# Performance work log

Hardware: AMD Instinct MI355X
Metric: run time of the kernel (lower is better)

The kernel has to match this reference:

```python
import jax, jax.numpy as jnp
import numpy as np

DIM = 512
HEADS = 8
HEAD_DIM = DIM // HEADS
R = 2  # reduce_ratio
SCALE = HEAD_DIM ** -0.5


def setup_inputs() -> dict:
    key = jax.random.key(0)
    ks = jax.random.split(key, 8)
    bs, H, W = 4, 64, 64
    n = H * W
    std = 0.02
    x = jax.random.normal(ks[0], (bs, n, DIM), dtype=jnp.float32)
    q_w = jax.random.normal(ks[1], (DIM, DIM), dtype=jnp.float32) * std
    kv_w = jax.random.normal(ks[2], (DIM, 2 * DIM), dtype=jnp.float32) * std
    proj_w = jax.random.normal(ks[3], (DIM, DIM), dtype=jnp.float32) * std
    proj_b = jnp.zeros((DIM,), dtype=jnp.float32)
    # Conv2d(dim, dim, kernel=R, stride=R), kaiming-like init
    fan_out = R * R * DIM
    sr_w = jax.random.normal(ks[4], (DIM, DIM, R, R), dtype=jnp.float32) * np.sqrt(2.0 / fan_out)
    sr_b = jnp.zeros((DIM,), dtype=jnp.float32)
    ln_w = jnp.ones((DIM,), dtype=jnp.float32)
    ln_b = jnp.zeros((DIM,), dtype=jnp.float32)
    return {"x": x, "q_w": q_w, "kv_w": kv_w, "proj_w": proj_w, "proj_b": proj_b,
            "sr_w": sr_w, "sr_b": sr_b, "ln_w": ln_w, "ln_b": ln_b, "H": H, "W": W}


def _layernorm(x, w, b, eps=1e-5):
    mu = jnp.mean(x, axis=-1, keepdims=True)
    var = jnp.var(x, axis=-1, keepdims=True)
    return (x - mu) * jax.lax.rsqrt(var + eps) * w + b


def reference(x, q_w, kv_w, proj_w, proj_b, sr_w, sr_b, ln_w, ln_b, H, W):
    bs, n, ch = x.shape
    # q: (bs, heads, n, head_dim)
    q = (x @ q_w).reshape(bs, n, HEADS, HEAD_DIM).transpose(0, 2, 1, 3)
    # spatial reduction of kv source: strided conv + layernorm
    x_img = x.transpose(0, 2, 1).reshape(bs, ch, H, W)
    xr = jax.lax.conv_general_dilated(
        x_img, sr_w, window_strides=(R, R), padding='VALID',
        dimension_numbers=('NCHW', 'OIHW', 'NCHW')) + sr_b[None, :, None, None]
    xr = xr.reshape(bs, ch, -1).transpose(0, 2, 1)  # (bs, n_kv, ch)
    xr = _layernorm(xr, ln_w, ln_b)
    kv = xr @ kv_w  # (bs, n_kv, 2*ch)
    n_kv = kv.shape[1]
    kv = kv.reshape(bs, n_kv, 2, HEADS, HEAD_DIM).transpose(2, 0, 3, 1, 4)
    k, v = kv[0], kv[1]  # (bs, heads, n_kv, head_dim)
    att = jnp.einsum('bhqd,bhkd->bhqk', q, k) * SCALE
    att = jax.nn.softmax(att, axis=-1)
    net = jnp.einsum('bhqk,bhkd->bhqd', att, v)
    net = net.transpose(0, 2, 1, 3).reshape(bs, n, ch)
    return net @ proj_w + proj_b
```

## Files before the change

kernel.cpp:

```cpp
#include <hip/hip_runtime.h>
#include <cstdint>

#define HEADS 8
#define HD 64
#define NQ 4096
#define NKV 1024

typedef unsigned short u16;
typedef __attribute__((ext_vector_type(8))) short short8;
typedef __attribute__((ext_vector_type(4))) float f32x4;
typedef __attribute__((ext_vector_type(16))) float f32x16;

__device__ __forceinline__ u16 f2bf(float f){
  union { float f; unsigned u; } c; c.f = f;
  unsigned r = c.u + 0x7fffu + ((c.u >> 16) & 1u);
  return (u16)(r >> 16);
}
__device__ __forceinline__ unsigned pack2(float a, float b){
  return (unsigned)f2bf(a) | ((unsigned)f2bf(b) << 16);
}
__device__ __forceinline__ float fexp2(float x){
  float r;
  asm("v_exp_f32 %0, %1" : "=v"(r) : "v"(x));
  return r;
}
__device__ __forceinline__ unsigned cvtpk(float a, float b){
  unsigned r;
  asm("v_cvt_pk_bf16_f32 %0, %1, %2" : "=v"(r) : "v"(a), "v"(b));
  return r;
}
__device__ __forceinline__ void gll16(const void* g, void* l){
  __builtin_amdgcn_global_load_lds((const __attribute__((address_space(1))) unsigned*)g,
                                   (__attribute__((address_space(3))) unsigned*)l, 16, 0, 0);
}
#define SB0() __builtin_amdgcn_sched_barrier(0)
#define MFMA16(a, b, c) __builtin_amdgcn_mfma_f32_16x16x32_bf16(a, b, c, 0, 0, 0)
#define MFMA32(a, b, c) __builtin_amdgcn_mfma_f32_32x32x16_bf16(a, b, c, 0, 0, 0)
#define Z16 {0.f,0.f,0.f,0.f,0.f,0.f,0.f,0.f,0.f,0.f,0.f,0.f,0.f,0.f,0.f,0.f}

__global__ __launch_bounds__(256) void prep_x(const float* __restrict__ x,
                                              u16* __restrict__ x_bf,
                                              u16* __restrict__ a_conv){
  int tid = blockIdx.x * 256 + threadIdx.x;
  int b   = tid >> 18;
  int rem = tid & 262143;
  int pos = rem >> 6;
  int ci0 = (rem & 63) << 3;
  size_t src = ((size_t)(b * NQ + pos)) * 512 + ci0;
  const float4* s4 = (const float4*)(x + src);
  float4 v0 = s4[0], v1 = s4[1];
  uint4 p;
  p.x = pack2(v0.x, v0.y); p.y = pack2(v0.z, v0.w);
  p.z = pack2(v1.x, v1.y); p.w = pack2(v1.z, v1.w);
  *(uint4*)(x_bf + src) = p;
  int h = pos >> 6, w = pos & 63;
  int pr = (h >> 1) * 32 + (w >> 1);
  int t  = (h & 1) * 2 + (w & 1);
  *(uint4*)(a_conv + ((size_t)(b * NKV + pr)) * 2048 + t * 512 + ci0) = p;
}

__global__ __launch_bounds__(256) void prep_w(const float* __restrict__ q_w,
                                              const float* __restrict__ kv_w,
                                              const float* __restrict__ proj_w,
                                              const float* __restrict__ sr_w,
                                              u16* __restrict__ q_wT, u16* __restrict__ kv_wT,
                                              u16* __restrict__ proj_wT, u16* __restrict__ conv_BT){
  int e = blockIdx.x * 256 + threadIdx.x;
  if (e < 262144){ int n = e >> 9, k = e & 511; q_wT[e] = f2bf(q_w[k * 512 + n]); return; }
  e -= 262144;
  if (e < 524288){ int n = e >> 9, k = e & 511; kv_wT[e] = f2bf(kv_w[k * 1024 + n]); return; }
  e -= 524288;
  if (e < 262144){ int n = e >> 9, k = e & 511; proj_wT[e] = f2bf(proj_w[k * 512 + n]); return; }
  e -= 262144;
  { int co = e >> 11, r = e & 2047, t = r >> 9, ci = r & 511;
    conv_BT[e] = f2bf(sr_w[co * 2048 + ci * 4 + t]); }
}

template<int MODE>
__global__ __launch_bounds__(256) void gemm_bt(const u16* __restrict__ A, const u16* __restrict__ BT,
                                               float* __restrict__ Cf, float* __restrict__ Cf2,
                                               u16* __restrict__ Cb0,
                                               u16* __restrict__ Cb1, const float* __restrict__ bias,
                                               int M, int N, int K){
  __shared__ __align__(16) u16 As[128 * 64];
  __shared__ __align__(16) u16 Bs[128 * 64];
  const int tid = threadIdx.x, lane = tid & 63, wave = tid >> 6;
  const int l15 = lane & 15, g = lane >> 4, r7 = l15 & 7;
  const int m0 = blockIdx.y * 128, n0 = blockIdx.x * 128;
  const int wr = wave >> 1, wc = wave & 1;
  const int kz = blockIdx.z;
  const int klen = K / (int)gridDim.z;
  const int kb = kz * klen;
  f32x4 acc[4][4] = {};
  for (int kt = kb; kt < kb + klen; kt += 64){
    #pragma unroll
    for (int i = 0; i < 4; ++i){
      int c = i * 256 + tid;
      int row = c >> 3, sc = (c & 7) ^ (row & 7);
      gll16(A  + (size_t)(m0 + row) * K + kt + sc * 8, As + (size_t)(i * 256 + wave * 64) * 8);
      gll16(BT + (size_t)(n0 + row) * K + kt + sc * 8, Bs + (size_t)(i * 256 + wave * 64) * 8);
    }
    __syncthreads();
    #pragma unroll
    for (int kk = 0; kk < 2; ++kk){
      short8 af[4];
      #pragma unroll
      for (int mi = 0; mi < 4; ++mi)
        af[mi] = *(const short8*)(As + (wr * 64 + mi * 16 + l15) * 64 + (((kk * 4 + g) ^ r7) << 3));
      #pragma unroll
      for (int ni = 0; ni < 4; ++ni){
        short8 bf = *(const short8*)(Bs + (wc * 64 + ni * 16 + l15) * 64 + (((kk * 4 + g) ^ r7) << 3));
        #pragma unroll
        for (int mi = 0; mi < 4; ++mi)
          acc[mi][ni] = MFMA16(af[mi], bf, acc[mi][ni]);
      }
    }
    __syncthreads();
  }
  #pragma unroll
  for (int mi = 0; mi < 4; ++mi){
    int row = m0 + wr * 64 + mi * 16 + (lane >> 4) * 4;
    #pragma unroll
    for (int ni = 0; ni < 4; ++ni){
      int col = n0 + wc * 64 + ni * 16 + l15;
      f32x4 v = acc[mi][ni];
      if (MODE == 0){
        float* Co = (kz < 2) ? (Cf + (size_t)kz * M * N) : (Cf2 + (size_t)(kz - 2) * M * N);
        float bb = (bias && kz == 0) ? bias[col] : 0.f;
        #pragma unroll
        for (int j = 0; j < 4; ++j) Co[(size_t)(row + j) * N + col] = v[j] + bb;
      } else if (MODE == 1){
        int h = col >> 6, d = col & 63;
        #pragma unroll
        for (int j = 0; j < 4; ++j){
          int r = row + j, b = r >> 12, nq = r & 4095;
          Cb0[(((size_t)(b * HEADS + h)) * NQ + nq) * HD + d] = f2bf(v[j] * 0.18033688f);
        }
      } else {
        int s = col >> 9, h = (col >> 6) & 7, d = col & 63;
        if (s == 0){
          #pragma unroll
          for (int j = 0; j < 4; ++j){
            int r = row + j, b = r >> 10, p = r & 1023;
            Cb0[(((size_t)(b * HEADS + h)) * NKV + p) * HD + d] = f2bf(v[j]);
          }
        } else {
          int b = row >> 10, p0 = row & 1023;
          int pp = (p0 & ~12) | (((p0 >> 2) & 1) << 3) | (((p0 >> 3) & 1) << 2);
          ushort4 pk;
          pk.x = f2bf(v[0]); pk.y = f2bf(v[1]); pk.z = f2bf(v[2]); pk.w = f2bf(v[3]);
          *(ushort4*)(Cb1 + (((size_t)(b * HEADS + h)) * HD + d) * NKV + pp) = pk;
        }
      }
    }
  }
}

__global__ __launch_bounds__(256) void ln_k(const float* __restrict__ xp, const float* __restrict__ xp2,
                                            const float* __restrict__ w,
                                            const float* __restrict__ bias, u16* __restrict__ xr){
  int row = blockIdx.x * 4 + (threadIdx.x >> 6);
  int lane = threadIdx.x & 63;
  const float* s1 = xp  + (size_t)row * 512;
  const float* s2 = s1 + (size_t)4096 * 512;
  const float* s3 = xp2 + (size_t)row * 512;
  const float* s4 = s3 + (size_t)4096 * 512;
  float vals[8]; float s = 0.f, ss = 0.f;
  #pragma unroll
  for (int j = 0; j < 8; ++j){
    int c = lane + j * 64;
    float v = (s1[c] + s2[c]) + (s3[c] + s4[c]);
    vals[j] = v; s += v; ss += v * v;
  }
  #pragma unroll
  for (int off = 32; off >= 1; off >>= 1){ s += __shfl_xor(s, off); ss += __shfl_xor(ss, off); }
  float mean = s * (1.f / 512.f);
  float var  = ss * (1.f / 512.f) - mean * mean;
  float rs = rsqrtf(var + 1e-5f);
  u16* dst = xr + (size_t)row * 512;
  #pragma unroll
  for (int j = 0; j < 8; ++j){
    int c = lane + j * 64;
    dst[c] = f2bf((vals[j] - mean) * rs * w[c] + bias[c]);
  }
}

template<bool LAST>
__device__ __forceinline__ void attn_tile(const u16* ksb, const u16* vsb,
                                          u16* kstage, u16* vstage,
                                          const u16* akg, const u16* avg,
                                          const short8* qf,
                                          int l31, int hi, int x7,
                                          f32x16* o, float& l_run){
  SB0();
  if (!LAST){
    gll16(akg,              kstage);
    gll16(akg + 2048,       kstage + 2048);
    gll16(avg,              vstage);
    gll16(avg + 32 * 1024,  vstage + 2048);
    SB0();
    asm volatile("s_waitcnt vmcnt(4)" ::: "memory");
  } else {
    asm volatile("s_waitcnt vmcnt(0)" ::: "memory");
  }
  __builtin_amdgcn_s_barrier();
  SB0();

  f32x16 sa[2];
  __builtin_amdgcn_s_setprio(1);
  #pragma unroll
  for (int sub = 0; sub < 2; ++sub){
    f32x16 a = Z16;
    #pragma unroll
    for (int ks = 0; ks < 4; ++ks){
      short8 kf = *(const short8*)(ksb + (sub * 32 + l31) * 64 + (((ks * 2 + hi) ^ x7) << 3));
      a = MFMA32(kf, qf[ks], a);
    }
    sa[sub] = a;
  }
  __builtin_amdgcn_s_setprio(0);

  unsigned w[16];
  float ps = 0.f;
  #pragma unroll
  for (int sub = 0; sub < 2; ++sub)
    #pragma unroll
    for (int t = 0; t < 8; ++t){
      float p0 = fexp2(sa[sub][2 * t]), p1 = fexp2(sa[sub][2 * t + 1]);
      ps += p0 + p1;
      w[sub * 8 + t] = cvtpk(p0, p1);
    }
  l_run += ps;

  __builtin_amdgcn_s_setprio(1);
  #pragma unroll
  for (int dt = 0; dt < 2; ++dt)
    #pragma unroll
    for (int sl = 0; sl < 4; ++sl){
      short8 vf = *(const short8*)(vsb + (dt * 32 + l31) * 64 + (((sl * 2 + hi) ^ x7) << 3));
      union { unsigned u[4]; short8 s; } bb;
      bb.u[0] = w[sl * 4 + 0]; bb.u[1] = w[sl * 4 + 1];
      bb.u[2] = w[sl * 4 + 2]; bb.u[3] = w[sl * 4 + 3];
      o[dt] = MFMA32(vf, bb.s, o[dt]);
    }
  __builtin_amdgcn_s_setprio(0);
  SB0();
  __builtin_amdgcn_s_barrier();
}

__global__ __launch_bounds__(256) void attn_k(const u16* __restrict__ q_s, const u16* __restrict__ k_s,
                                              const u16* __restrict__ vt_s, u16* __restrict__ net){
  __shared__ __align__(16) u16 Ks[2][64 * 64];
  __shared__ __align__(16) u16 Vt[2][64 * 64];
  const int tid = threadIdx.x, lane = tid & 63, wave = tid >> 6;
  const int l31 = lane & 31, hi = lane >> 5, x7 = lane & 7;
  const int bh = blockIdx.y;
  const u16* kb  = k_s  + (size_t)bh * NKV * HD;
  const u16* vtb = vt_s + (size_t)bh * HD * NKV;
  const int q0 = blockIdx.x * 128 + wave * 32;
  const u16* qbase = q_s + ((size_t)bh * NQ + q0 + l31) * HD + hi * 8;
  short8 qf[4];
  #pragma unroll
  for (int ks = 0; ks < 4; ++ks) qf[ks] = *(const short8*)(qbase + ks * 16);

  const int swz8 = (((tid & 7) ^ ((tid >> 3) & 7)) << 3);
  const u16* ak0 = kb  + (size_t)(tid >> 3) * 64   + swz8;
  const u16* av0 = vtb + (size_t)(tid >> 3) * 1024 + swz8;

  f32x16 o[2] = { Z16, Z16 };
  float l_run = 0.f;

  gll16(ak0,             &Ks[0][wave * 512]);
  gll16(ak0 + 2048,      &Ks[0][2048 + wave * 512]);
  gll16(av0,             &Vt[0][wave * 512]);
  gll16(av0 + 32 * 1024, &Vt[0][2048 + wave * 512]);

  for (int tt = 0; tt < 7; ++tt){
    attn_tile<false>(&Ks[0][0], &Vt[0][0], &Ks[1][wave * 512], &Vt[1][wave * 512],
                     ak0 + (size_t)(2 * tt + 1) * 4096, av0 + (2 * tt + 1) * 64,
                     qf, l31, hi, x7, o, l_run);
    attn_tile<false>(&Ks[1][0], &Vt[1][0], &Ks[0][wave * 512], &Vt[0][wave * 512],
                     ak0 + (size_t)(2 * tt + 2) * 4096, av0 + (2 * tt + 2) * 64,
                     qf, l31, hi, x7, o, l_run);
  }
  attn_tile<false>(&Ks[0][0], &Vt[0][0], &Ks[1][wave * 512], &Vt[1][wave * 512],
                   ak0 + (size_t)15 * 4096, av0 + 15 * 64,
                   qf, l31, hi, x7, o, l_run);
  attn_tile<true>(&Ks[1][0], &Vt[1][0], nullptr, nullptr, nullptr, nullptr,
                  qf, l31, hi, x7, o, l_run);

  float l = l_run + __shfl_xor(l_run, 32);
  float inv = 1.f / l;
  int b = bh >> 3, h = bh & 7;
  size_t obase = ((size_t)b * NQ + q0 + l31) * 512 + h * 64;
  #pragma unroll
  for (int dt = 0; dt < 2; ++dt)
    #pragma unroll
    for (int t = 0; t < 8; ++t){
      int j = 2 * t;
      int d = dt * 32 + (j & 3) + 8 * (j >> 2) + 4 * hi;
      *(unsigned*)(net + obase + d) = cvtpk(o[dt][j] * inv, o[dt][j + 1] * inv);
    }
}

extern "C" void kernel_launch(void* const* d_in, const int* in_sizes, int n_in,
                              void* d_out, int out_size, void* d_ws, size_t ws_size,
                              hipStream_t stream){
  const float* x      = (const float*)d_in[0];
  const float* q_w    = (const float*)d_in[1];
  const float* kv_w   = (const float*)d_in[2];
  const float* proj_w = (const float*)d_in[3];
  const float* proj_b = (const float*)d_in[4];
  const float* sr_w   = (const float*)d_in[5];
  const float* sr_b   = (const float*)d_in[6];
  const float* ln_w   = (const float*)d_in[7];
  const float* ln_b   = (const float*)d_in[8];
  (void)in_sizes; (void)n_in; (void)out_size; (void)ws_size;

  char* ws = (char*)d_ws;
  u16*   x_bf    = (u16*)(ws);
  float* xr_pre2 = (float*)(ws);
  u16*   a_conv  = (u16*)(ws + ((size_t)16 << 20));
  u16*   xr      = (u16*)(ws + ((size_t)16 << 20));
  u16*   net     = (u16*)(ws + ((size_t)16 << 20));
  u16*   q_sb    = (u16*)(ws + ((size_t)32 << 20));
  float* xr_pre  = (float*)(ws + ((size_t)48 << 20));
  u16*   k_sb    = (u16*)(ws + ((size_t)48 << 20));
  u16*   vt_sb   = (u16*)(ws + ((size_t)52 << 20));
  u16*   q_wT    = (u16*)(ws + ((size_t)64 << 20));
  u16*   kv_wT   = (u16*)(ws + ((size_t)64 << 20) + 524288);
  u16*   proj_wT = (u16*)(ws + ((size_t)64 << 20) + 524288 + 1048576);
  u16*   conv_BT = (u16*)(ws + ((size_t)64 << 20) + 524288 + 1048576 + 524288);
  float* out = (float*)d_out;

  prep_w<<<8192, 256, 0, stream>>>(q_w, kv_w, proj_w, sr_w, q_wT, kv_wT, proj_wT, conv_BT);
  prep_x<<<4096, 256, 0, stream>>>(x, x_bf, a_conv);
  gemm_bt<1><<<dim3(4, 128), 256, 0, stream>>>(x_bf, q_wT, nullptr, nullptr, q_sb, nullptr, nullptr, 16384, 512, 512);
  gemm_bt<0><<<dim3(4, 32, 4), 256, 0, stream>>>(a_conv, conv_BT, xr_pre, xr_pre2, nullptr, nullptr, sr_b, 4096, 512, 2048);
  ln_k<<<1024, 256, 0, stream>>>(xr_pre, xr_pre2, ln_w, ln_b, xr);
  gemm_bt<2><<<dim3(8, 32),  256, 0, stream>>>(xr, kv_wT, nullptr, nullptr, k_sb, vt_sb, nullptr, 4096, 1024, 512);
  attn_k<<<dim3(32, 32), 256, 0, stream>>>(q_sb, k_sb, vt_sb, net);
  gemm_bt<0><<<dim3(4, 128), 256, 0, stream>>>(net, proj_wT, out, nullptr, nullptr, nullptr, proj_b, 16384, 512, 512);
}
```

Baseline: 147.5 us.

## Merge prep and GEMM launches, reorder attention sync, remap blocks to XCDs

Merges the two prep kernels into one launch, and merges the Q projection GEMM with the split-K conv GEMM into one launch selected by blockIdx.y. In the attention tile loop, the sync point moves so the wait and barrier come before the QK^T MFMAs, and the next-tile prefetch is issued after them; the trailing barrier is dropped. Attention blocks are remapped to a 1D grid so each XCD handles four (batch, head) pairs, which should improve L2 reuse of K/V. The result is fewer launches and better locality, but removing the trailing barrier risks a race on the double-buffered LDS stage.

```diff
diff --git a/kernel.cpp b/kernel.cpp
--- a/kernel.cpp
+++ b/kernel.cpp
@@ -38,34 +38,36 @@
 #define MFMA32(a, b, c) __builtin_amdgcn_mfma_f32_32x32x16_bf16(a, b, c, 0, 0, 0)
 #define Z16 {0.f,0.f,0.f,0.f,0.f,0.f,0.f,0.f,0.f,0.f,0.f,0.f,0.f,0.f,0.f,0.f}
 
-__global__ __launch_bounds__(256) void prep_x(const float* __restrict__ x,
-                                              u16* __restrict__ x_bf,
-                                              u16* __restrict__ a_conv){
-  int tid = blockIdx.x * 256 + threadIdx.x;
-  int b   = tid >> 18;
-  int rem = tid & 262143;
-  int pos = rem >> 6;
-  int ci0 = (rem & 63) << 3;
-  size_t src = ((size_t)(b * NQ + pos)) * 512 + ci0;
-  const float4* s4 = (const float4*)(x + src);
-  float4 v0 = s4[0], v1 = s4[1];
-  uint4 p;
-  p.x = pack2(v0.x, v0.y); p.y = pack2(v0.z, v0.w);
-  p.z = pack2(v1.x, v1.y); p.w = pack2(v1.z, v1.w);
-  *(uint4*)(x_bf + src) = p;
-  int h = pos >> 6, w = pos & 63;
-  int pr = (h >> 1) * 32 + (w >> 1);
-  int t  = (h & 1) * 2 + (w & 1);
-  *(uint4*)(a_conv + ((size_t)(b * NKV + pr)) * 2048 + t * 512 + ci0) = p;
-}
-
-__global__ __launch_bounds__(256) void prep_w(const float* __restrict__ q_w,
-                                              const float* __restrict__ kv_w,
-                                              const float* __restrict__ proj_w,
-                                              const float* __restrict__ sr_w,
-                                              u16* __restrict__ q_wT, u16* __restrict__ kv_wT,
-                                              u16* __restrict__ proj_wT, u16* __restrict__ conv_BT){
-  int e = blockIdx.x * 256 + threadIdx.x;
+__global__ __launch_bounds__(256) void prep_all(const float* __restrict__ x,
+                                                const float* __restrict__ q_w,
+                                                const float* __restrict__ kv_w,
+                                                const float* __restrict__ proj_w,
+                                                const float* __restrict__ sr_w,
+                                                u16* __restrict__ x_bf,
+                                                u16* __restrict__ a_conv,
+                                                u16* __restrict__ q_wT, u16* __restrict__ kv_wT,
+                                                u16* __restrict__ proj_wT, u16* __restrict__ conv_BT){
+  int bid = blockIdx.x;
+  if (bid < 4096){
+    int tid = bid * 256 + threadIdx.x;
+    int b   = tid >> 18;
+    int rem = tid & 262143;
+    int pos = rem >> 6;
+    int ci0 = (rem & 63) << 3;
+    size_t src = ((size_t)(b * NQ + pos)) * 512 + ci0;
+    const float4* s4 = (const float4*)(x + src);
+    float4 v0 = s4[0], v1 = s4[1];
+    uint4 p;
+    p.x = pack2(v0.x, v0.y); p.y = pack2(v0.z, v0.w);
+    p.z = pack2(v1.x, v1.y); p.w = pack2(v1.z, v1.w);
+    *(uint4*)(x_bf + src) = p;
+    int h = pos >> 6, w = pos & 63;
+    int pr = (h >> 1) * 32 + (w >> 1);
+    int t  = (h & 1) * 2 + (w & 1);
+    *(uint4*)(a_conv + ((size_t)(b * NKV + pr)) * 2048 + t * 512 + ci0) = p;
+    return;
+  }
+  int e = (bid - 4096) * 256 + threadIdx.x;
   if (e < 262144){ int n = e >> 9, k = e & 511; q_wT[e] = f2bf(q_w[k * 512 + n]); return; }
   e -= 262144;
   if (e < 524288){ int n = e >> 9, k = e & 511; kv_wT[e] = f2bf(kv_w[k * 1024 + n]); return; }
@@ -76,29 +78,32 @@
     conv_BT[e] = f2bf(sr_w[co * 2048 + ci * 4 + t]); }
 }
 
-template<int MODE>
-__global__ __launch_bounds__(256) void gemm_bt(const u16* __restrict__ A, const u16* __restrict__ BT,
-                                               float* __restrict__ Cf, float* __restrict__ Cf2,
-                                               u16* __restrict__ Cb0,
-                                               u16* __restrict__ Cb1, const float* __restrict__ bias,
-                                               int M, int N, int K){
+__global__ __launch_bounds__(256) void gemm_qconv(const u16* __restrict__ x_bf, const u16* __restrict__ q_wT,
+                                                  const u16* __restrict__ a_conv, const u16* __restrict__ conv_BT,
+                                                  u16* __restrict__ q_sb, float* __restrict__ xr_pre,
+                                                  float* __restrict__ xr_pre2, const float* __restrict__ sr_b){
   __shared__ __align__(16) u16 As[128 * 64];
   __shared__ __align__(16) u16 Bs[128 * 64];
   const int tid = threadIdx.x, lane = tid & 63, wave = tid >> 6;
   const int l15 = lane & 15, g = lane >> 4, r7 = l15 & 7;
-  const int m0 = blockIdx.y * 128, n0 = blockIdx.x * 128;
   const int wr = wave >> 1, wc = wave & 1;
-  const int kz = blockIdx.z;
-  const int klen = K / (int)gridDim.z;
-  const int kb = kz * klen;
+  int y = blockIdx.y;
+  const u16 *A, *BT;
+  int K, kb, m0, kz = 0;
+  bool isQ;
+  if (y < 128){ isQ = true;  A = x_bf;   BT = q_wT;    K = 512;  kb = 0;       m0 = y * 128; }
+  else { y -= 128; kz = y >> 5;
+         isQ = false; A = a_conv; BT = conv_BT; K = 2048; kb = kz << 9; m0 = (y & 31) * 128; }
+  const int n0 = blockIdx.x * 128;
   f32x4 acc[4][4] = {};
-  for (int kt = kb; kt < kb + klen; kt += 64){
-    #pragma unroll
-    for (int i = 0; i < 4; ++i){
-      int c = i * 256 + tid;
+  for (int i = 0; i < 8; ++i){
+    int kt = kb + i * 64;
+    #pragma unroll
+    for (int ii = 0; ii < 4; ++ii){
+      int c = ii * 256 + tid;
       int row = c >> 3, sc = (c & 7) ^ (row & 7);
-      gll16(A  + (size_t)(m0 + row) * K + kt + sc * 8, As + (size_t)(i * 256 + wave * 64) * 8);
-      gll16(BT + (size_t)(n0 + row) * K + kt + sc * 8, Bs + (size_t)(i * 256 + wave * 64) * 8);
+      gll16(A  + (size_t)(m0 + row) * K + kt + sc * 8, As + (size_t)(ii * 256 + wave * 64) * 8);
+      gll16(BT + (size_t)(n0 + row) * K + kt + sc * 8, Bs + (size_t)(ii * 256 + wave * 64) * 8);
     }
     __syncthreads();
     #pragma unroll
@@ -124,18 +129,73 @@
     for (int ni = 0; ni < 4; ++ni){
       int col = n0 + wc * 64 + ni * 16 + l15;
       f32x4 v = acc[mi][ni];
-      if (MODE == 0){
-        float* Co = (kz < 2) ? (Cf + (size_t)kz * M * N) : (Cf2 + (size_t)(kz - 2) * M * N);
-        float bb = (bias && kz == 0) ? bias[col] : 0.f;
-        #pragma unroll
-        for (int j = 0; j < 4; ++j) Co[(size_t)(row + j) * N + col] = v[j] + bb;
-      } else if (MODE == 1){
+      if (isQ){
         int h = col >> 6, d = col & 63;
         #pragma unroll
         for (int j = 0; j < 4; ++j){
           int r = row + j, b = r >> 12, nq = r & 4095;
-          Cb0[(((size_t)(b * HEADS + h)) * NQ + nq) * HD + d] = f2bf(v[j] * 0.18033688f);
+          q_sb[(((size_t)(b * HEADS + h)) * NQ + nq) * HD + d] = f2bf(v[j] * 0.18033688f);
         }
+      } else {
+        float* Co = (kz < 2) ? (xr_pre + (size_t)kz * 4096 * 512)
+                             : (xr_pre2 + (size_t)(kz - 2) * 4096 * 512);
+        float bb = (kz == 0) ? sr_b[col] : 0.f;
+        #pragma unroll
+        for (int j = 0; j < 4; ++j) Co[(size_t)(row + j) * 512 + col] = v[j] + bb;
+      }
+    }
+  }
+}
+
+template<int MODE>
+__global__ __launch_bounds__(256) void gemm_bt(const u16* __restrict__ A, const u16* __restrict__ BT,
+                                               float* __restrict__ Cf,
+                                               u16* __restrict__ Cb0,
+                                               u16* __restrict__ Cb1, const float* __restrict__ bias,
+                                               int M, int N, int K){
+  __shared__ __align__(16) u16 As[128 * 64];
+  __shared__ __align__(16) u16 Bs[128 * 64];
+  const int tid = threadIdx.x, lane = tid & 63, wave = tid >> 6;
+  const int l15 = lane & 15, g = lane >> 4, r7 = l15 & 7;
+  const int m0 = blockIdx.y * 128, n0 = blockIdx.x * 128;
+  const int wr = wave >> 1, wc = wave & 1;
+  f32x4 acc[4][4] = {};
+  for (int kt = 0; kt < K; kt += 64){
+    #pragma unroll
+    for (int i = 0; i < 4; ++i){
+      int c = i * 256 + tid;
+      int row = c >> 3, sc = (c & 7) ^ (row & 7);
+      gll16(A  + (size_t)(m0 + row) * K + kt + sc * 8, As + (size_t)(i * 256 + wave * 64) * 8);
+      gll16(BT + (size_t)(n0 + row) * K + kt + sc * 8, Bs + (size_t)(i * 256 + wave * 64) * 8);
+    }
+    __syncthreads();
+    #pragma unroll
+    for (int kk = 0; kk < 2; ++kk){
+      short8 af[4];
+      #pragma unroll
+      for (int mi = 0; mi < 4; ++mi)
+        af[mi] = *(const short8*)(As + (wr * 64 + mi * 16 + l15) * 64 + (((kk * 4 + g) ^ r7) << 3));
+      #pragma unroll
+      for (int ni = 0; ni < 4; ++ni){
+        short8 bf = *(const short8*)(Bs + (wc * 64 + ni * 16 + l15) * 64 + (((kk * 4 + g) ^ r7) << 3));
+        #pragma unroll
+        for (int mi = 0; mi < 4; ++mi)
+          acc[mi][ni] = MFMA16(af[mi], bf, acc[mi][ni]);
+      }
+    }
+    __syncthreads();
+  }
+  #pragma unroll
+  for (int mi = 0; mi < 4; ++mi){
+    int row = m0 + wr * 64 + mi * 16 + (lane >> 4) * 4;
+    #pragma unroll
+    for (int ni = 0; ni < 4; ++ni){
+      int col = n0 + wc * 64 + ni * 16 + l15;
+      f32x4 v = acc[mi][ni];
+      if (MODE == 0){
+        float bb = bias ? bias[col] : 0.f;
+        #pragma unroll
+        for (int j = 0; j < 4; ++j) Cf[(size_t)(row + j) * N + col] = v[j] + bb;
       } else {
         int s = col >> 9, h = (col >> 6) & 7, d = col & 63;
         if (s == 0){
@@ -192,33 +252,32 @@
                                           const short8* qf,
                                           int l31, int hi, int x7,
                                           f32x16* o, float& l_run){
+  asm volatile("s_waitcnt vmcnt(0)" ::: "memory");
+  __builtin_amdgcn_s_barrier();
   SB0();
+
+  f32x16 sa[2];
+  __builtin_amdgcn_s_setprio(1);
+  #pragma unroll
+  for (int sub = 0; sub < 2; ++sub){
+    f32x16 a = Z16;
+    #pragma unroll
+    for (int ks = 0; ks < 4; ++ks){
+      short8 kf = *(const short8*)(ksb + (sub * 32 + l31) * 64 + (((ks * 2 + hi) ^ x7) << 3));
+      a = MFMA32(kf, qf[ks], a);
+    }
+    sa[sub] = a;
+  }
+  __builtin_amdgcn_s_setprio(0);
+  SB0();
+
   if (!LAST){
     gll16(akg,              kstage);
     gll16(akg + 2048,       kstage + 2048);
     gll16(avg,              vstage);
     gll16(avg + 32 * 1024,  vstage + 2048);
-    SB0();
-    asm volatile("s_waitcnt vmcnt(4)" ::: "memory");
-  } else {
-    asm volatile("s_waitcnt vmcnt(0)" ::: "memory");
-  }
-  __builtin_amdgcn_s_barrier();
+  }
   SB0();
-
-  f32x16 sa[2];
-  __builtin_amdgcn_s_setprio(1);
-  #pragma unroll
-  for (int sub = 0; sub < 2; ++sub){
-    f32x16 a = Z16;
-    #pragma unroll
-    for (int ks = 0; ks < 4; ++ks){
-      short8 kf = *(const short8*)(ksb + (sub * 32 + l31) * 64 + (((ks * 2 + hi) ^ x7) << 3));
-      a = MFMA32(kf, qf[ks], a);
-    }
-    sa[sub] = a;
-  }
-  __builtin_amdgcn_s_setprio(0);
 
   unsigned w[16];
   float ps = 0.f;
@@ -245,7 +304,6 @@
     }
   __builtin_amdgcn_s_setprio(0);
   SB0();
-  __builtin_amdgcn_s_barrier();
 }
 
 __global__ __launch_bounds__(256) void attn_k(const u16* __restrict__ q_s, const u16* __restrict__ k_s,
@@ -254,10 +312,13 @@
   __shared__ __align__(16) u16 Vt[2][64 * 64];
   const int tid = threadIdx.x, lane = tid & 63, wave = tid >> 6;
   const int l31 = lane & 31, hi = lane >> 5, x7 = lane & 7;
-  const int bh = blockIdx.y;
+  const int id = blockIdx.x;
+  const int xcd = id & 7, slot = id >> 3;
+  const int bh = 4 * xcd + (slot >> 5);
+  const int qblk = slot & 31;
   const u16* kb  = k_s  + (size_t)bh * NKV * HD;
   const u16* vtb = vt_s + (size_t)bh * HD * NKV;
-  const int q0 = blockIdx.x * 128 + wave * 32;
+  const int q0 = qblk * 128 + wave * 32;
   const u16* qbase = q_s + ((size_t)bh * NQ + q0 + l31) * HD + hi * 8;
   short8 qf[4];
   #pragma unroll
@@ -333,12 +394,12 @@
   u16*   conv_BT = (u16*)(ws + ((size_t)64 << 20) + 524288 + 1048576 + 524288);
   float* out = (float*)d_out;
 
-  prep_w<<<8192, 256, 0, stream>>>(q_w, kv_w, proj_w, sr_w, q_wT, kv_wT, proj_wT, conv_BT);
-  prep_x<<<4096, 256, 0, stream>>>(x, x_bf, a_conv);
-  gemm_bt<1><<<dim3(4, 128), 256, 0, stream>>>(x_bf, q_wT, nullptr, nullptr, q_sb, nullptr, nullptr, 16384, 512, 512);
-  gemm_bt<0><<<dim3(4, 32, 4), 256, 0, stream>>>(a_conv, conv_BT, xr_pre, xr_pre2, nullptr, nullptr, sr_b, 4096, 512, 2048);
+  prep_all<<<12288, 256, 0, stream>>>(x, q_w, kv_w, proj_w, sr_w,
+                                      x_bf, a_conv, q_wT, kv_wT, proj_wT, conv_BT);
+  gemm_qconv<<<dim3(4, 256), 256, 0, stream>>>(x_bf, q_wT, a_conv, conv_BT,
+                                               q_sb, xr_pre, xr_pre2, sr_b);
   ln_k<<<1024, 256, 0, stream>>>(xr_pre, xr_pre2, ln_w, ln_b, xr);
-  gemm_bt<2><<<dim3(8, 32),  256, 0, stream>>>(xr, kv_wT, nullptr, nullptr, k_sb, vt_sb, nullptr, 4096, 1024, 512);
-  attn_k<<<dim3(32, 32), 256, 0, stream>>>(q_sb, k_sb, vt_sb, net);
-  gemm_bt<0><<<dim3(4, 128), 256, 0, stream>>>(net, proj_wT, out, nullptr, nullptr, nullptr, proj_b, 16384, 512, 512);
-}
+  gemm_bt<2><<<dim3(8, 32),  256, 0, stream>>>(xr, kv_wT, nullptr, k_sb, vt_sb, nullptr, 4096, 1024, 512);
+  attn_k<<<1024, 256, 0, stream>>>(q_sb, k_sb, vt_sb, net);
+  gemm_bt<0><<<dim3(4, 128), 256, 0, stream>>>(net, proj_wT, out, nullptr, nullptr, proj_b, 16384, 512, 512);
+}
```

Result: faster. 143.3 us (-2.9%).
